# Performance work log

Measured on AMD Instinct MI355X. Metric: run time of the kernel, lower is better.

Reference implementation:

```python
import jax, jax.numpy as jnp
import numpy as np

N_C, N_F = 25000, 100000   # coarse / fine node counts
E_C, E_F = 100000, 400000  # coarse / fine edge counts
W, F_IN, F_OUT = 128, 128, 4


def _fnn2(x, w1, b1, w2, b2):
    # 2-layer FNN (fnns_depth=2) with SELU, dropout=0 (eval)
    return jax.nn.selu(x @ w1 + b1) @ w2 + b2


def _interaction(v, e, src, dst, n, ew1, eb1, ew2, eb2, nw1, nb1, nw2, nb2):
    # InteractionNetwork: edge update (gather) -> mean scatter -> node update, residuals
    e = _fnn2(jnp.concatenate([e, v[src], v[dst]], axis=-1), ew1, eb1, ew2, eb2) + e
    s = jax.ops.segment_sum(e, dst, num_segments=n)
    cnt = jax.ops.segment_sum(jnp.ones((e.shape[0], 1), e.dtype), dst, num_segments=n)
    agg = s / jnp.maximum(cnt, 1.0)  # 'mean' aggregation
    v = _fnn2(jnp.concatenate([v, agg], axis=-1), nw1, nb1, nw2, nb2) + v
    return v, e


def setup_inputs() -> dict:
    key = jax.random.key(0)
    ks = iter(jax.random.split(key, 64))
    def rn(shape, scale=1.0):
        return jax.random.normal(next(ks), shape, jnp.float32) * scale
    s3, s2, s1 = 1.0 / np.sqrt(3 * W), 1.0 / np.sqrt(2 * W), 1.0 / np.sqrt(W)
    d = {
        'v': rn((N_C, F_IN)),
        'c_coarse': rn((N_C, W)), 'c_fine': rn((N_F, W)),
        'e_coarse': rn((E_C, W)), 'e_fine': rn((E_F, W)),
        'rel_dist': rn((N_F, 1)),
        'ei_coarse': jax.random.randint(next(ks), (2, E_C), 0, N_C),
        'ei_fine': jax.random.randint(next(ks), (2, E_F), 0, N_F),
        'cluster': jax.random.randint(next(ks), (N_F,), 0, N_C),
        'in_node_w': rn((F_IN, W), 1.0 / np.sqrt(F_IN)), 'in_node_b': rn((W,), 0.01),
        'cond_w': rn((2, W, W), s1), 'cond_b': rn((2, W), 0.01),
        'edge_in_w': rn((2, W, W), s1), 'edge_in_b': rn((2, W), 0.01),
        'bn_ew1': rn((2, 3 * W, W), s3), 'bn_eb1': rn((2, W), 0.01),
        'bn_ew2': rn((2, W, W), s1), 'bn_eb2': rn((2, W), 0.01),
        'bn_nw1': rn((2, 2 * W, W), s2), 'bn_nb1': rn((2, W), 0.01),
        'bn_nw2': rn((2, W, W), s1), 'bn_nb2': rn((2, W), 0.01),
        'unp_w1': rn((W + 1, W), 1.0 / np.sqrt(W + 1)), 'unp_b1': rn((W,), 0.01),
        'unp_w2': rn((W, W), s1), 'unp_b2': rn((W,), 0.01),
        'up_ew1': rn((2, 3 * W, W), s3), 'up_eb1': rn((2, W), 0.01),
        'up_ew2': rn((2, W, W), s1), 'up_eb2': rn((2, W), 0.01),
        'up_nw1': rn((2, 2 * W, W), s2), 'up_nb1': rn((2, W), 0.01),
        'up_nw2': rn((2, W, W), s1), 'up_nb2': rn((2, W), 0.01),
        'out_w': rn((W, F_OUT), s1), 'out_b': rn((F_OUT,), 0.01),
    }
    return d


def reference(v, c_coarse, c_fine, e_coarse, e_fine, rel_dist, ei_coarse, ei_fine, cluster,
              in_node_w, in_node_b, cond_w, cond_b, edge_in_w, edge_in_b,
              bn_ew1, bn_eb1, bn_ew2, bn_eb2, bn_nw1, bn_nb1, bn_nw2, bn_nb2,
              unp_w1, unp_b1, unp_w2, unp_b2,
              up_ew1, up_eb1, up_ew2, up_eb2, up_nw1, up_nb1, up_nw2, up_nb2,
              out_w, out_b):
    src_c, dst_c = ei_coarse[0], ei_coarse[1]
    src_f, dst_f = ei_fine[0], ei_fine[1]
    # input projection + coarse-scale conditioning
    v = v @ in_node_w + in_node_b
    v = v + (c_coarse @ cond_w[0] + cond_b[0])
    e = e_coarse @ edge_in_w[0] + edge_in_b[0]
    # bottleneck InteractionNetwork blocks on coarse graph
    for i in range(bn_ew1.shape[0]):
        v, e = _interaction(v, e, src_c, dst_c, N_C,
                            bn_ew1[i], bn_eb1[i], bn_ew2[i], bn_eb2[i],
                            bn_nw1[i], bn_nb1[i], bn_nw2[i], bn_nb2[i])
    # up block: project skip conditioning/edges, unpool coarse->fine via cluster gather + FNN on [v, scalar rel pos]
    c = c_fine @ cond_w[1] + cond_b[1]
    e = e_fine @ edge_in_w[1] + edge_in_b[1]
    v = _fnn2(jnp.concatenate([v[cluster], rel_dist], axis=-1), unp_w1, unp_b1, unp_w2, unp_b2)
    v = v + c
    for i in range(up_ew1.shape[0]):
        v, e = _interaction(v, e, src_f, dst_f, N_F,
                            up_ew1[i], up_eb1[i], up_ew2[i], up_eb2[i],
                            up_nw1[i], up_nb1[i], up_nw2[i], up_nb2[i])
    return v @ out_w + out_b
```

## Files before the change

kernel.cpp:

```cpp
#include <hip/hip_runtime.h>
#include <hip/hip_bf16.h>

typedef __bf16 bf16_t;
typedef __bf16 bf16x8 __attribute__((ext_vector_type(8)));
typedef float f32x4 __attribute__((ext_vector_type(4)));

#define SELU_SCALE 1.0507009873554805f
#define SELU_ALPHA 1.6732632423543772f

__device__ __forceinline__ float selu_f(float x) {
    return x > 0.0f ? SELU_SCALE * x : SELU_SCALE * SELU_ALPHA * (__expf(x) - 1.0f);
}

__device__ __forceinline__ int4 load8(const void* p, size_t elem_off, int isf) {
    if (!isf) return *(const int4*)((const bf16_t*)p + elem_off);
    const float* f = (const float*)p + elem_off;
    float4 a = ((const float4*)f)[0], b = ((const float4*)f)[1];
    union { int4 i; bf16_t h[8]; } u;
    u.h[0] = (bf16_t)a.x; u.h[1] = (bf16_t)a.y; u.h[2] = (bf16_t)a.z; u.h[3] = (bf16_t)a.w;
    u.h[4] = (bf16_t)b.x; u.h[5] = (bf16_t)b.y; u.h[6] = (bf16_t)b.z; u.h[7] = (bf16_t)b.w;
    return u.i;
}

__global__ void detect_dtype(const unsigned short* p, int* flag) {
    if (threadIdx.x == 0) {
        float m = 0.0f;
        for (int i = 0; i < 128; i++) {
            unsigned int u = ((unsigned int)p[i]) << 16;
            float v = __uint_as_float(u);
            v = fabsf(v);
            if (!(v <= 1e3f)) { m = 1e30f; break; }
            m = fmaxf(m, v);
        }
        *flag = (m > 1e3f) ? 1 : 0;
    }
}

struct VDesc { const void* s; bf16_t* d; int eoff; int n; };
struct VArgs { VDesc v[19]; };
__global__ void convert_vecs(VArgs a, const int* __restrict__ flag) {
    int isf = *flag;
    VDesc vd = a.v[blockIdx.y];
    int i = blockIdx.x * 256 + threadIdx.x;
    if (i < vd.n) {
        size_t idx = (size_t)vd.eoff + i;
        vd.d[i] = isf ? (bf16_t)(((const float*)vd.s)[idx]) : ((const bf16_t*)vd.s)[idx];
    }
}

struct TDesc { const void* s; bf16_t* d; int eoff; int Ksrc; int Ktot; int koff; };
struct TArgs { TDesc t[31]; };
__global__ void transpose_all(TArgs a, const int* __restrict__ flag) {
    int isf = *flag;
    TDesc td = a.t[blockIdx.y];
    int i = blockIdx.x * 256 + threadIdx.x;
    if (i < 128 * td.Ksrc) {
        int n = i / td.Ksrc;
        int k = i - n * td.Ksrc;
        size_t si = (size_t)td.eoff + (size_t)k * 128 + n;
        bf16_t v = isf ? (bf16_t)(((const float*)td.s)[si]) : ((const bf16_t*)td.s)[si];
        td.d[(size_t)n * td.Ktot + td.koff + k] = v;
    }
}

__global__ void count_dst2(const int* __restrict__ d0, int* __restrict__ c0, int E0,
                           const int* __restrict__ d1, int* __restrict__ c1, int E1) {
    const int* dst = blockIdx.y ? d1 : d0;
    int* cnt = blockIdx.y ? c1 : c0;
    int E = blockIdx.y ? E1 : E0;
    int e = blockIdx.x * 256 + threadIdx.x;
    if (e < E) atomicAdd(&cnt[dst[e]], 1);
}

__global__ void seg_alloc2(const int* __restrict__ c0, int* __restrict__ rp0, int* __restrict__ cu0, int n0,
                           const int* __restrict__ c1, int* __restrict__ rp1, int* __restrict__ cu1, int n1,
                           int* __restrict__ totals) {
    const int* cnt = blockIdx.y ? c1 : c0;
    int* rp = blockIdx.y ? rp1 : rp0;
    int* cu = blockIdx.y ? cu1 : cu0;
    int n = blockIdx.y ? n1 : n0;
    int* total = totals + blockIdx.y;
    int i = blockIdx.x * 256 + threadIdx.x;
    if (i < n) { int s = atomicAdd(total, cnt[i]); rp[i] = s; cu[i] = s; }
}

__global__ void csr_scatter2(const int* __restrict__ d0, int* __restrict__ cu0, int* __restrict__ e0, int E0,
                             const int* __restrict__ d1, int* __restrict__ cu1, int* __restrict__ e1, int E1) {
    const int* dst = blockIdx.y ? d1 : d0;
    int* cur = blockIdx.y ? cu1 : cu0;
    int* eids = blockIdx.y ? e1 : e0;
    int E = blockIdx.y ? E1 : E0;
    int e = blockIdx.x * 256 + threadIdx.x;
    if (e < E) {
        unsigned s = (unsigned)atomicAdd(&cur[dst[e]], 1);
        if (s < (unsigned)E) eids[s] = e;
    }
}

template<int K, int N>
__global__ __launch_bounds__(256) void lin1(
    int M, const void* __restrict__ A0, const void* __restrict__ A1,
    const bf16_t* __restrict__ Wt, const bf16_t* __restrict__ b1,
    const bf16_t* __restrict__ b2, const bf16_t* __restrict__ res,
    bf16_t* __restrict__ out, const int* __restrict__ flag)
{
    constexpr int SA = K + 8;
    constexpr int NCT = N / 64;
    __shared__ bf16_t sA[64 * SA];
    const int isf = *flag;
    const int tid = threadIdx.x;
    const int row0 = blockIdx.x * 64;
    const int lane16 = tid & 15;
    const int rgrp = tid >> 4;

    #pragma unroll
    for (int chunk = 0; chunk < K; chunk += 128) {
        const void* sp = chunk ? A1 : A0;
        for (int r = rgrp; r < 64; r += 16) {
            int rr = row0 + r; if (rr >= M) rr = M - 1;
            int4 u = load8(sp, (size_t)rr * 128 + lane16 * 8, isf);
            *(int4*)&sA[r * SA + chunk + lane16 * 8] = u;
        }
    }
    __syncthreads();

    const int lane = tid & 63, wave = tid >> 6;
    const int l15 = lane & 15, lk = lane >> 4;
    const int colbase = wave * (N / 4);
    f32x4 acc[4][NCT];
    const f32x4 zero = {0.f, 0.f, 0.f, 0.f};
    for (int rt = 0; rt < 4; rt++)
        for (int ct = 0; ct < NCT; ct++) acc[rt][ct] = zero;

    #pragma unroll
    for (int k0 = 0; k0 < K; k0 += 32) {
        bf16x8 wv[NCT];
        #pragma unroll
        for (int ct = 0; ct < NCT; ct++)
            wv[ct] = *(const bf16x8*)(Wt + (size_t)(colbase + ct * 16 + l15) * K + k0 + lk * 8);
        #pragma unroll
        for (int rt = 0; rt < 4; rt++) {
            bf16x8 av = *(const bf16x8*)(&sA[(rt * 16 + l15) * SA + k0 + lk * 8]);
            #pragma unroll
            for (int ct = 0; ct < NCT; ct++)
                acc[rt][ct] = __builtin_amdgcn_mfma_f32_16x16x32_bf16(av, wv[ct], acc[rt][ct], 0, 0, 0);
        }
    }

    #pragma unroll
    for (int rt = 0; rt < 4; rt++)
        #pragma unroll
        for (int ct = 0; ct < NCT; ct++) {
            int col = colbase + ct * 16 + l15;
            float bc = (float)b1[col] + (b2 ? (float)b2[col] : 0.0f);
            #pragma unroll
            for (int r = 0; r < 4; r++) {
                int grow = row0 + rt * 16 + lk * 4 + r;
                if (grow < M) {
                    float x = acc[rt][ct][r] + bc;
                    if (res) x += (float)res[(size_t)grow * N + col];
                    out[(size_t)grow * N + col] = (bf16_t)x;
                }
            }
        }
}

template<int MODE>
__global__ __launch_bounds__(512, 8) void fnn2k(
    int M,
    const bf16_t* __restrict__ A0, const bf16_t* __restrict__ Psd,
    const int* __restrict__ g0, const int* __restrict__ g1,
    const bf16_t* __restrict__ Emat, const int* __restrict__ rp,
    const int* __restrict__ degc, const int* __restrict__ eids,
    const bf16_t* __restrict__ W1t, const bf16_t* __restrict__ b1,
    const bf16_t* __restrict__ W2t, const bf16_t* __restrict__ b2,
    const bf16_t* __restrict__ relb, const bf16_t* __restrict__ w1last,
    const bf16_t* __restrict__ res, bf16_t* __restrict__ out,
    const bf16_t* __restrict__ finw, const bf16_t* __restrict__ finb,
    void* __restrict__ fout, const int* __restrict__ flag)
{
    constexpr int NP = (MODE == 3) ? 1 : 2;
    constexpr int K1 = (MODE == 2) ? 256 : 128;
    constexpr int PL = 64 * 136;
    __shared__ bf16_t sA[NP * PL];
    bf16_t* sH = sA + (NP - 1) * PL;

    const int isf = *flag;
    const int tid = threadIdx.x;
    const int lane16 = tid & 15;
    const int rgrp = tid >> 4;
    const int lane = tid & 63, wave = tid >> 6;
    const int l15 = lane & 15, lk = lane >> 4;
    const int colbase = wave * 16;
    const int row0 = blockIdx.x * 64;
    const bool res_lds = (res == A0);
    const f32x4 zero = {0.f, 0.f, 0.f, 0.f};

    #pragma unroll
    for (int c = 0; c < NP; c++) {
        #pragma unroll
        for (int i = 0; i < 2; i++) {
            int r = rgrp + i * 32;
            int rr = row0 + r; if (rr >= M) rr = M - 1;
            int4 u;
            if (MODE == 1 && c == 1) {
                bf16x8 pa = *(const bf16x8*)(Psd + (size_t)g0[rr] * 256 + lane16 * 8);
                bf16x8 pb = *(const bf16x8*)(Psd + (size_t)g1[rr] * 256 + 128 + lane16 * 8);
                union { int4 i4; bf16_t h[8]; } w;
                #pragma unroll
                for (int j = 0; j < 8; j++) w.h[j] = (bf16_t)((float)pa[j] + (float)pb[j]);
                u = w.i4;
            } else if (MODE == 2 && c == 1) {
                int beg = rp[rr], deg = degc[rr];
                float a8[8] = {0.f, 0.f, 0.f, 0.f, 0.f, 0.f, 0.f, 0.f};
                for (int e = 0; e < deg; e++) {
                    int eid = eids[beg + e];
                    bf16x8 ev = *(const bf16x8*)(Emat + (size_t)eid * 128 + lane16 * 8);
                    #pragma unroll
                    for (int j = 0; j < 8; j++) a8[j] += (float)ev[j];
                }
                float inv = 1.0f / (float)(deg > 0 ? deg : 1);
                union { int4 i4; bf16_t h[8]; } w;
                #pragma unroll
                for (int j = 0; j < 8; j++) w.h[j] = (bf16_t)(a8[j] * inv);
                u = w.i4;
            } else {
                const bf16_t* sp = (MODE == 3) ? A0 + (size_t)g0[rr] * 128
                                               : A0 + (size_t)rr * 128;
                u = *(const int4*)(sp + lane16 * 8);
            }
            *(int4*)&sA[c * PL + r * 136 + lane16 * 8] = u;
        }
    }
    __syncthreads();

    f32x4 acc[4];
    #pragma unroll
    for (int rt = 0; rt < 4; rt++) acc[rt] = zero;
    #pragma unroll
    for (int k0 = 0; k0 < K1; k0 += 32) {
        bf16x8 w0 = *(const bf16x8*)(W1t + (size_t)(colbase + l15) * K1 + k0 + lk * 8);
        #pragma unroll
        for (int rt = 0; rt < 4; rt++) {
            bf16x8 av = *(const bf16x8*)(&sA[(k0 / 128) * PL + (rt * 16 + l15) * 136 + (k0 & 127) + lk * 8]);
            acc[rt] = __builtin_amdgcn_mfma_f32_16x16x32_bf16(av, w0, acc[rt], 0, 0, 0);
        }
    }
    if (MODE != 1) __syncthreads();

    {
        int col = colbase + l15;
        float b1c = (float)b1[col];
        float wlc = (MODE == 3) ? (float)w1last[col] : 0.0f;
        #pragma unroll
        for (int rt = 0; rt < 4; rt++)
            #pragma unroll
            for (int r = 0; r < 4; r++) {
                int lrow = rt * 16 + lk * 4 + r;
                int grow = row0 + lrow;
                float x = acc[rt][r] + b1c;
                if (MODE == 1) x += (float)sH[lrow * 136 + col];
                if (MODE == 3) {
                    float rv = (grow < M) ? (float)relb[grow] : 0.0f;
                    x += rv * wlc;
                }
                x = selu_f(x);
                sH[lrow * 136 + col] = (bf16_t)x;
            }
    }
    __syncthreads();

    f32x4 acc2[4];
    #pragma unroll
    for (int rt = 0; rt < 4; rt++) acc2[rt] = zero;
    #pragma unroll
    for (int k0 = 0; k0 < 128; k0 += 32) {
        bf16x8 w0 = *(const bf16x8*)(W2t + (size_t)(colbase + l15) * 128 + k0 + lk * 8);
        #pragma unroll
        for (int rt = 0; rt < 4; rt++) {
            bf16x8 av = *(const bf16x8*)(&sH[(rt * 16 + l15) * 136 + k0 + lk * 8]);
            acc2[rt] = __builtin_amdgcn_mfma_f32_16x16x32_bf16(av, w0, acc2[rt], 0, 0, 0);
        }
    }
    if (finw) __syncthreads();

    {
        int col = colbase + l15;
        float b2c = (float)b2[col];
        #pragma unroll
        for (int rt = 0; rt < 4; rt++)
            #pragma unroll
            for (int r = 0; r < 4; r++) {
                int lrow = rt * 16 + lk * 4 + r;
                int grow = row0 + lrow;
                if (grow < M) {
                    float x = acc2[rt][r] + b2c;
                    if (res) {
                        float rv = (res_lds && NP > 1) ? (float)sA[lrow * 136 + col]
                                                       : (float)res[(size_t)grow * 128 + col];
                        x += rv;
                    }
                    bf16_t xb = (bf16_t)x;
                    if (out) out[(size_t)grow * 128 + col] = xb;
                    if (finw) sH[lrow * 136 + col] = xb;
                }
            }
    }

    if (finw) {
        __syncthreads();
        if (tid < 256) {
            int orow = tid >> 2, c = tid & 3;
            int grow = row0 + orow;
            if (grow < M) {
                float s = (float)finb[c];
                #pragma unroll
                for (int k = 0; k < 128; k++)
                    s += (float)sH[orow * 136 + k] * (float)finw[k * 4 + c];
                if (isf) ((float*)fout)[(size_t)grow * 4 + c] = s;
                else     ((bf16_t*)fout)[(size_t)grow * 4 + c] = (bf16_t)s;
            }
        }
    }
}

extern "C" void kernel_launch(void* const* d_in, const int* in_sizes, int n_in,
                              void* d_out, int out_size, void* d_ws, size_t ws_size,
                              hipStream_t stream) {
    const int NC = 25000, NF = 100000, EC = 100000, EF = 400000;

    const void* v_in      = d_in[0];
    const void* c_coarse  = d_in[1];
    const void* c_fine    = d_in[2];
    const void* e_coarse  = d_in[3];
    const void* e_fine    = d_in[4];
    const void* rel_dist  = d_in[5];
    const int*  ei_c      = (const int*)d_in[6];
    const int*  ei_f      = (const int*)d_in[7];
    const int*  cluster   = (const int*)d_in[8];
    const void* in_node_w = d_in[9];
    const void* in_node_b = d_in[10];
    const void* cond_w    = d_in[11];
    const void* cond_b    = d_in[12];
    const void* edge_in_w = d_in[13];
    const void* edge_in_b = d_in[14];
    const void* bn_ew1    = d_in[15];
    const void* bn_eb1    = d_in[16];
    const void* bn_ew2    = d_in[17];
    const void* bn_eb2    = d_in[18];
    const void* bn_nw1    = d_in[19];
    const void* bn_nb1    = d_in[20];
    const void* bn_nw2    = d_in[21];
    const void* bn_nb2    = d_in[22];
    const void* unp_w1    = d_in[23];
    const void* unp_b1    = d_in[24];
    const void* unp_w2    = d_in[25];
    const void* unp_b2    = d_in[26];
    const void* up_ew1    = d_in[27];
    const void* up_eb1    = d_in[28];
    const void* up_ew2    = d_in[29];
    const void* up_eb2    = d_in[30];
    const void* up_nw1    = d_in[31];
    const void* up_nb1    = d_in[32];
    const void* up_nw2    = d_in[33];
    const void* up_nb2    = d_in[34];
    const void* out_w     = d_in[35];
    const void* out_b     = d_in[36];

    const int* src_c = ei_c, * dst_c = ei_c + EC;
    const int* src_f = ei_f, * dst_f = ei_f + EF;

    char* base = (char*)d_ws;
    size_t off = 0;
    auto carve = [&](size_t bytes) -> void* {
        void* p = base + off;
        off += (bytes + 255) & ~(size_t)255;
        return p;
    };
    int*    flag   = (int*)carve(256);
    int*    zflag  = (int*)carve(256);
    int*    totals = (int*)carve(256);
    bf16_t* vc     = (bf16_t*)carve((size_t)NC * 128 * 2);
    bf16_t* vf     = (bf16_t*)carve((size_t)NF * 128 * 2);
    bf16_t* ef     = (bf16_t*)carve((size_t)EF * 128 * 2);
    bf16_t* ec     = ef;
    bf16_t* Psd    = (bf16_t*)carve((size_t)NF * 256 * 2);
    int*    cnti_c = (int*)carve((size_t)NC * 4);
    int*    cnti_f = (int*)carve((size_t)NF * 4);
    int*    rp_c   = (int*)carve((size_t)NC * 4);
    int*    rp_f   = (int*)carve((size_t)NF * 4);
    int*    cur_c  = (int*)carve((size_t)NC * 4);
    int*    cur_f  = (int*)carve((size_t)NF * 4);

    auto cw = [&](size_t elems) -> bf16_t* { return (bf16_t*)carve(elems * 2); };
    bf16_t* Wic    = cw(128 * 256);
    bf16_t* Wein0  = cw(128 * 128);
    bf16_t* Wein1  = cw(128 * 128);
    bf16_t* Wcond1 = cw(128 * 128);
    bf16_t* Wbe1[2] = { cw(128 * 128), cw(128 * 128) };
    bf16_t* Wsd_c[2] = { cw(256 * 128), cw(256 * 128) };
    bf16_t* Wbe2[2] = { cw(128 * 128), cw(128 * 128) };
    bf16_t* Wbn1[2] = { cw(128 * 256), cw(128 * 256) };
    bf16_t* Wbn2[2] = { cw(128 * 128), cw(128 * 128) };
    bf16_t* Wunp1 = cw(128 * 128);
    bf16_t* Wunp2 = cw(128 * 128);
    bf16_t* Wue1[2] = { cw(128 * 128), cw(128 * 128) };
    bf16_t* Wsd_f[2] = { cw(256 * 128), cw(256 * 128) };
    bf16_t* Wue2[2] = { cw(128 * 128), cw(128 * 128) };
    bf16_t* Wun1[2] = { cw(128 * 256), cw(128 * 256) };
    bf16_t* Wun2[2] = { cw(128 * 128), cw(128 * 128) };
    bf16_t* b_in   = cw(128);
    bf16_t* b_cond = cw(256);
    bf16_t* b_ein  = cw(256);
    bf16_t* b_be1  = cw(256);
    bf16_t* b_be2  = cw(256);
    bf16_t* b_bn1  = cw(256);
    bf16_t* b_bn2  = cw(256);
    bf16_t* b_unp1 = cw(128);
    bf16_t* b_unp2 = cw(128);
    bf16_t* b_ue1  = cw(256);
    bf16_t* b_ue2  = cw(256);
    bf16_t* b_un1  = cw(256);
    bf16_t* b_un2  = cw(256);
    bf16_t* b_out  = cw(8);
    bf16_t* w1last = cw(128);
    bf16_t* relb   = cw(NF);
    bf16_t* foutw  = cw(512);
    bf16_t* zerob  = cw(256);
    int*    eids_c = (int*)carve((size_t)EC * 4);
    int*    eids_f = (int*)carve((size_t)EF * 4);

    detect_dtype<<<1, 64, 0, stream>>>((const unsigned short*)in_node_b, flag);
    hipMemsetAsync(zflag, 0, 256, stream);
    hipMemsetAsync(zerob, 0, 512, stream);

    VArgs va; int vi = 0;
    auto addV = [&](const void* s, bf16_t* d, int eoff, int n) {
        va.v[vi].s = s; va.v[vi].d = d; va.v[vi].eoff = eoff; va.v[vi].n = n; vi++;
    };
    addV(in_node_b, b_in, 0, 128);
    addV(cond_b, b_cond, 0, 256);
    addV(edge_in_b, b_ein, 0, 256);
    addV(bn_eb1, b_be1, 0, 256);  addV(bn_eb2, b_be2, 0, 256);
    addV(bn_nb1, b_bn1, 0, 256);  addV(bn_nb2, b_bn2, 0, 256);
    addV(unp_b1, b_unp1, 0, 128); addV(unp_b2, b_unp2, 0, 128);
    addV(up_eb1, b_ue1, 0, 256);  addV(up_eb2, b_ue2, 0, 256);
    addV(up_nb1, b_un1, 0, 256);  addV(up_nb2, b_un2, 0, 256);
    addV(out_b, b_out, 0, 4);
    addV(unp_w1, w1last, 128 * 128, 128);
    addV(rel_dist, relb, 0, NF);
    addV(out_w, foutw, 0, 512);
    dim3 vg((NF + 255) / 256, vi);
    convert_vecs<<<vg, 256, 0, stream>>>(va, flag);

    TArgs ta; int ti = 0;
    auto addT = [&](const void* s, bf16_t* d, int eoff, int Ksrc, int Ktot, int koff) {
        ta.t[ti].s = s; ta.t[ti].d = d; ta.t[ti].eoff = eoff;
        ta.t[ti].Ksrc = Ksrc; ta.t[ti].Ktot = Ktot; ta.t[ti].koff = koff; ti++;
    };
    addT(in_node_w, Wic, 0, 128, 256, 0);
    addT(cond_w,    Wic, 0, 128, 256, 128);
    addT(edge_in_w, Wein0, 0, 128, 128, 0);
    addT(edge_in_w, Wein1, 16384, 128, 128, 0);
    addT(cond_w,    Wcond1, 16384, 128, 128, 0);
    for (int i = 0; i < 2; i++) {
        addT(bn_ew1, Wbe1[i],           i * 49152,         128, 128, 0);
        addT(bn_ew1, Wsd_c[i],          i * 49152 + 16384, 128, 128, 0);
        addT(bn_ew1, Wsd_c[i] + 16384,  i * 49152 + 32768, 128, 128, 0);
        addT(bn_ew2, Wbe2[i], i * 16384, 128, 128, 0);
        addT(bn_nw1, Wbn1[i], i * 32768, 256, 256, 0);
        addT(bn_nw2, Wbn2[i], i * 16384, 128, 128, 0);
        addT(up_ew1, Wue1[i],           i * 49152,         128, 128, 0);
        addT(up_ew1, Wsd_f[i],          i * 49152 + 16384, 128, 128, 0);
        addT(up_ew1, Wsd_f[i] + 16384,  i * 49152 + 32768, 128, 128, 0);
        addT(up_ew2, Wue2[i], i * 16384, 128, 128, 0);
        addT(up_nw1, Wun1[i], i * 32768, 256, 256, 0);
        addT(up_nw2, Wun2[i], i * 16384, 128, 128, 0);
    }
    addT(unp_w1, Wunp1, 0, 128, 128, 0);
    addT(unp_w2, Wunp2, 0, 128, 128, 0);
    dim3 tg((128 * 256 + 255) / 256, ti);
    transpose_all<<<tg, 256, 0, stream>>>(ta, flag);

    hipMemsetAsync(cnti_c, 0, (size_t)NC * 4, stream);
    hipMemsetAsync(cnti_f, 0, (size_t)NF * 4, stream);
    hipMemsetAsync(totals, 0, 256, stream);
    dim3 ge((EF + 255) / 256, 2), gn((NF + 255) / 256, 2);
    count_dst2<<<ge, 256, 0, stream>>>(dst_c, cnti_c, EC, dst_f, cnti_f, EF);
    seg_alloc2<<<gn, 256, 0, stream>>>(cnti_c, rp_c, cur_c, NC, cnti_f, rp_f, cur_f, NF, totals);
    csr_scatter2<<<ge, 256, 0, stream>>>(dst_c, cur_c, eids_c, EC, dst_f, cur_f, eids_f, EF);

    lin1<256, 128><<<(NC + 63) / 64, 256, 0, stream>>>(NC, v_in, c_coarse, Wic, b_in, b_cond,
                                                       nullptr, vc, flag);
    lin1<128, 128><<<(EC + 63) / 64, 256, 0, stream>>>(EC, e_coarse, nullptr, Wein0, b_ein,
                                                       nullptr, nullptr, ec, flag);

    for (int i = 0; i < 2; i++) {
        lin1<128, 256><<<(NC + 63) / 64, 256, 0, stream>>>(NC, vc, nullptr, Wsd_c[i], zerob,
                                                           nullptr, nullptr, Psd, zflag);
        fnn2k<1><<<(EC + 63) / 64, 512, 0, stream>>>(
            EC, ec, Psd, src_c, dst_c, nullptr, nullptr, nullptr, nullptr,
            Wbe1[i], b_be1 + i * 128, Wbe2[i], b_be2 + i * 128,
            nullptr, nullptr, ec, ec, nullptr, nullptr, nullptr, flag);
        fnn2k<2><<<(NC + 63) / 64, 512, 0, stream>>>(
            NC, vc, nullptr, nullptr, nullptr, ec, rp_c, cnti_c, eids_c,
            Wbn1[i], b_bn1 + i * 128, Wbn2[i], b_bn2 + i * 128,
            nullptr, nullptr, vc, vc, nullptr, nullptr, nullptr, flag);
    }

    lin1<128, 128><<<(NF + 63) / 64, 256, 0, stream>>>(NF, c_fine, nullptr, Wcond1, b_cond + 128,
                                                       nullptr, nullptr, vf, flag);
    fnn2k<3><<<(NF + 63) / 64, 512, 0, stream>>>(
        NF, vc, nullptr, cluster, nullptr, nullptr, nullptr, nullptr, nullptr,
        Wunp1, b_unp1, Wunp2, b_unp2,
        relb, w1last, vf, vf, nullptr, nullptr, nullptr, flag);
    lin1<128, 128><<<(EF + 63) / 64, 256, 0, stream>>>(EF, e_fine, nullptr, Wein1, b_ein + 128,
                                                       nullptr, nullptr, ef, flag);

    for (int i = 0; i < 2; i++) {
        lin1<128, 256><<<(NF + 63) / 64, 256, 0, stream>>>(NF, vf, nullptr, Wsd_f[i], zerob,
                                                           nullptr, nullptr, Psd, zflag);
        fnn2k<1><<<(EF + 63) / 64, 512, 0, stream>>>(
            EF, ef, Psd, src_f, dst_f, nullptr, nullptr, nullptr, nullptr,
            Wue1[i], b_ue1 + i * 128, Wue2[i], b_ue2 + i * 128,
            nullptr, nullptr, ef, ef, nullptr, nullptr, nullptr, flag);
        int last = (i == 1);
        fnn2k<2><<<(NF + 63) / 64, 512, 0, stream>>>(
            NF, vf, nullptr, nullptr, nullptr, ef, rp_f, cnti_f, eids_f,
            Wun1[i], b_un1 + i * 128, Wun2[i], b_un2 + i * 128,
            nullptr, nullptr, vf, (last ? nullptr : vf),
            (last ? foutw : nullptr), b_out,
            (last ? d_out : nullptr), flag);
    }
}
```

Baseline: 794.9 us.

## Store edge features in destination-sorted CSR order for contiguous aggregation

Result: no change. 782.6 us (-1.5%).

```diff
diff --git a/kernel.cpp b/kernel.cpp
--- a/kernel.cpp
+++ b/kernel.cpp
@@ -97,9 +97,26 @@
     }
 }
 
+__global__ void permute_ends2(const int* __restrict__ e0, const int* __restrict__ s0,
+                              const int* __restrict__ d0, int* __restrict__ sp0,
+                              int* __restrict__ dp0, int E0,
+                              const int* __restrict__ e1, const int* __restrict__ s1,
+                              const int* __restrict__ d1, int* __restrict__ sp1,
+                              int* __restrict__ dp1, int E1) {
+    const int* eids = blockIdx.y ? e1 : e0;
+    const int* src = blockIdx.y ? s1 : s0;
+    const int* dst = blockIdx.y ? d1 : d0;
+    int* sp = blockIdx.y ? sp1 : sp0;
+    int* dp = blockIdx.y ? dp1 : dp0;
+    int E = blockIdx.y ? E1 : E0;
+    int s = blockIdx.x * 256 + threadIdx.x;
+    if (s < E) { int e = eids[s]; sp[s] = src[e]; dp[s] = dst[e]; }
+}
+
 template<int K, int N>
 __global__ __launch_bounds__(256) void lin1(
     int M, const void* __restrict__ A0, const void* __restrict__ A1,
+    const int* __restrict__ gi,
     const bf16_t* __restrict__ Wt, const bf16_t* __restrict__ b1,
     const bf16_t* __restrict__ b2, const bf16_t* __restrict__ res,
     bf16_t* __restrict__ out, const int* __restrict__ flag)
@@ -118,6 +135,7 @@
         const void* sp = chunk ? A1 : A0;
         for (int r = rgrp; r < 64; r += 16) {
             int rr = row0 + r; if (rr >= M) rr = M - 1;
+            if (gi) rr = gi[rr];
             int4 u = load8(sp, (size_t)rr * 128 + lane16 * 8, isf);
             *(int4*)&sA[r * SA + chunk + lane16 * 8] = u;
         }
@@ -171,7 +189,7 @@
     const bf16_t* __restrict__ A0, const bf16_t* __restrict__ Psd,
     const int* __restrict__ g0, const int* __restrict__ g1,
     const bf16_t* __restrict__ Emat, const int* __restrict__ rp,
-    const int* __restrict__ degc, const int* __restrict__ eids,
+    const int* __restrict__ degc,
     const bf16_t* __restrict__ W1t, const bf16_t* __restrict__ b1,
     const bf16_t* __restrict__ W2t, const bf16_t* __restrict__ b2,
     const bf16_t* __restrict__ relb, const bf16_t* __restrict__ w1last,
@@ -213,9 +231,10 @@
             } else if (MODE == 2 && c == 1) {
                 int beg = rp[rr], deg = degc[rr];
                 float a8[8] = {0.f, 0.f, 0.f, 0.f, 0.f, 0.f, 0.f, 0.f};
+                const bf16_t* ep = Emat + (size_t)beg * 128 + lane16 * 8;
                 for (int e = 0; e < deg; e++) {
-                    int eid = eids[beg + e];
-                    bf16x8 ev = *(const bf16x8*)(Emat + (size_t)eid * 128 + lane16 * 8);
+                    bf16x8 ev = *(const bf16x8*)ep;
+                    ep += 128;
                     #pragma unroll
                     for (int j = 0; j < 8; j++) a8[j] += (float)ev[j];
                 }
@@ -391,6 +410,10 @@
     int*    rp_f   = (int*)carve((size_t)NF * 4);
     int*    cur_c  = (int*)carve((size_t)NC * 4);
     int*    cur_f  = (int*)carve((size_t)NF * 4);
+    int*    srcp_c = (int*)carve((size_t)EC * 4);
+    int*    dstp_c = (int*)carve((size_t)EC * 4);
+    int*    srcp_f = (int*)carve((size_t)EF * 4);
+    int*    dstp_f = (int*)carve((size_t)EF * 4);
 
     auto cw = [&](size_t elems) -> bf16_t* { return (bf16_t*)carve(elems * 2); };
     bf16_t* Wic    = cw(128 * 256);
@@ -489,44 +512,46 @@
     count_dst2<<<ge, 256, 0, stream>>>(dst_c, cnti_c, EC, dst_f, cnti_f, EF);
     seg_alloc2<<<gn, 256, 0, stream>>>(cnti_c, rp_c, cur_c, NC, cnti_f, rp_f, cur_f, NF, totals);
     csr_scatter2<<<ge, 256, 0, stream>>>(dst_c, cur_c, eids_c, EC, dst_f, cur_f, eids_f, EF);
-
-    lin1<256, 128><<<(NC + 63) / 64, 256, 0, stream>>>(NC, v_in, c_coarse, Wic, b_in, b_cond,
-                                                       nullptr, vc, flag);
-    lin1<128, 128><<<(EC + 63) / 64, 256, 0, stream>>>(EC, e_coarse, nullptr, Wein0, b_ein,
-                                                       nullptr, nullptr, ec, flag);
+    permute_ends2<<<ge, 256, 0, stream>>>(eids_c, src_c, dst_c, srcp_c, dstp_c, EC,
+                                          eids_f, src_f, dst_f, srcp_f, dstp_f, EF);
+
+    lin1<256, 128><<<(NC + 63) / 64, 256, 0, stream>>>(NC, v_in, c_coarse, nullptr, Wic,
+                                                       b_in, b_cond, nullptr, vc, flag);
+    lin1<128, 128><<<(EC + 63) / 64, 256, 0, stream>>>(EC, e_coarse, nullptr, eids_c, Wein0,
+                                                       b_ein, nullptr, nullptr, ec, flag);
 
     for (int i = 0; i < 2; i++) {
-        lin1<128, 256><<<(NC + 63) / 64, 256, 0, stream>>>(NC, vc, nullptr, Wsd_c[i], zerob,
-                                                           nullptr, nullptr, Psd, zflag);
+        lin1<128, 256><<<(NC + 63) / 64, 256, 0, stream>>>(NC, vc, nullptr, nullptr, Wsd_c[i],
+                                                           zerob, nullptr, nullptr, Psd, zflag);
         fnn2k<1><<<(EC + 63) / 64, 512, 0, stream>>>(
-            EC, ec, Psd, src_c, dst_c, nullptr, nullptr, nullptr, nullptr,
+            EC, ec, Psd, srcp_c, dstp_c, nullptr, nullptr, nullptr,
             Wbe1[i], b_be1 + i * 128, Wbe2[i], b_be2 + i * 128,
             nullptr, nullptr, ec, ec, nullptr, nullptr, nullptr, flag);
         fnn2k<2><<<(NC + 63) / 64, 512, 0, stream>>>(
-            NC, vc, nullptr, nullptr, nullptr, ec, rp_c, cnti_c, eids_c,
+            NC, vc, nullptr, nullptr, nullptr, ec, rp_c, cnti_c,
             Wbn1[i], b_bn1 + i * 128, Wbn2[i], b_bn2 + i * 128,
             nullptr, nullptr, vc, vc, nullptr, nullptr, nullptr, flag);
     }
 
-    lin1<128, 128><<<(NF + 63) / 64, 256, 0, stream>>>(NF, c_fine, nullptr, Wcond1, b_cond + 128,
-                                                       nullptr, nullptr, vf, flag);
+    lin1<128, 128><<<(NF + 63) / 64, 256, 0, stream>>>(NF, c_fine, nullptr, nullptr, Wcond1,
+                                                       b_cond + 128, nullptr, nullptr, vf, flag);
     fnn2k<3><<<(NF + 63) / 64, 512, 0, stream>>>(
-        NF, vc, nullptr, cluster, nullptr, nullptr, nullptr, nullptr, nullptr,
+        NF, vc, nullptr, cluster, nullptr, nullptr, nullptr, nullptr,
         Wunp1, b_unp1, Wunp2, b_unp2,
         relb, w1last, vf, vf, nullptr, nullptr, nullptr, flag);
-    lin1<128, 128><<<(EF + 63) / 64, 256, 0, stream>>>(EF, e_fine, nullptr, Wein1, b_ein + 128,
-                                                       nullptr, nullptr, ef, flag);
+    lin1<128, 128><<<(EF + 63) / 64, 256, 0, stream>>>(EF, e_fine, nullptr, eids_f, Wein1,
+                                                       b_ein + 128, nullptr, nullptr, ef, flag);
 
     for (int i = 0; i < 2; i++) {
-        lin1<128, 256><<<(NF + 63) / 64, 256, 0, stream>>>(NF, vf, nullptr, Wsd_f[i], zerob,
-                                                           nullptr, nullptr, Psd, zflag);
+        lin1<128, 256><<<(NF + 63) / 64, 256, 0, stream>>>(NF, vf, nullptr, nullptr, Wsd_f[i],
+                                                           zerob, nullptr, nullptr, Psd, zflag);
         fnn2k<1><<<(EF + 63) / 64, 512, 0, stream>>>(
-            EF, ef, Psd, src_f, dst_f, nullptr, nullptr, nullptr, nullptr,
+            EF, ef, Psd, srcp_f, dstp_f, nullptr, nullptr, nullptr,
             Wue1[i], b_ue1 + i * 128, Wue2[i], b_ue2 + i * 128,
             nullptr, nullptr, ef, ef, nullptr, nullptr, nullptr, flag);
         int last = (i == 1);
         fnn2k<2><<<(NF + 63) / 64, 512, 0, stream>>>(
-            NF, vf, nullptr, nullptr, nullptr, ef, rp_f, cnti_f, eids_f,
+            NF, vf, nullptr, nullptr, nullptr, ef, rp_f, cnti_f,
             Wun1[i], b_un1 + i * 128, Wun2[i], b_un2 + i * 128,
             nullptr, nullptr, vf, (last ? nullptr : vf),
             (last ? foutw : nullptr), b_out,
```
